# Performance work log

Measured on AMD Instinct MI355X. Metric: run time of the kernel, lower is better.

## Reference

```python
import jax, jax.numpy as jnp
import numpy as np

EPS = 1e-7
MAX_NORM = 1.0 - 1e-3  # projection radius of the unit Poincare ball (c=1)
ALPHA = 0.2            # LeakyReLU negative slope
NEG_INF = -9e15


def _proj(x, max_norm=MAX_NORM):
    # Project points back inside the Poincare ball along the last dim.
    norm = jnp.clip(jnp.linalg.norm(x, axis=-1, keepdims=True), EPS)
    return jnp.where(norm > max_norm, x / norm * max_norm, x)


def _logmap0(x):
    # Log map at the origin of the Poincare ball, c = 1.
    norm = jnp.clip(jnp.linalg.norm(x, axis=-1, keepdims=True), EPS, 1.0 - EPS)
    return jnp.arctanh(norm) * x / norm


def _expmap0(v):
    # Exp map at the origin of the Poincare ball, c = 1.
    norm = jnp.clip(jnp.linalg.norm(v, axis=-1, keepdims=True), EPS)
    return jnp.tanh(norm) * v / norm


def setup_inputs() -> dict:
    key = jax.random.key(0)
    k1, k2, k3 = jax.random.split(key, 3)
    N, D = 12288, 128
    # points strictly inside the ball: ||x|| ~ 0.01*sqrt(128) ~ 0.11 < 1
    x = jax.random.normal(k1, (N, D), dtype=jnp.float32) * 0.01
    adj = jax.random.randint(k2, (N, N), 0, 2, dtype=jnp.int32)
    # attention vector a, as in init: N(0, 0.2) then proj(a, 0.9) row-wise
    a = jax.random.normal(k3, (2 * D, 1), dtype=jnp.float32) * 0.2
    a = _proj(a, 0.9)
    return {"x": x, "adj": adj, "a": a}


def reference(x, adj, a):
    D = a.shape[0] // 2
    x_tan = _logmap0(x)                       # [N, D]
    wh1 = x_tan @ a[:D]                       # [N, 1]
    wh2 = x_tan @ a[D:]                       # [N, 1]
    e = jax.nn.leaky_relu(wh1 + wh2.T, ALPHA)  # [N, N] additive scores
    scores = jnp.where(adj > 0, e, NEG_INF)
    attention = jax.nn.softmax(scores, axis=1)  # dropout omitted (eval mode)
    x_tan_prime = attention @ x_tan            # [N, D]
    return _proj(_expmap0(x_tan_prime))
```

## Files before the change

kernel.cpp:

```cpp
#include <hip/hip_runtime.h>
#include <math.h>

#define NN 12288
#define DD 128
#define EPSF 1e-7f
#define MAXNORM (1.0f - 1e-3f)
#define S_SLABS 24

typedef __attribute__((ext_vector_type(8))) short short8_t;
typedef __attribute__((ext_vector_type(4))) float float4_t;
typedef unsigned short ushort_t;

__device__ __forceinline__ unsigned short f2bf(float f) {
    unsigned int u = __builtin_bit_cast(unsigned int, f);
    unsigned int r = u + 0x7FFFu + ((u >> 16) & 1u);
    return (unsigned short)(r >> 16);
}

__global__ __launch_bounds__(128) void prep_kernel(
    const float* __restrict__ x, const float* __restrict__ a,
    ushort_t* __restrict__ xtb,
    float* __restrict__ wh1, float* __restrict__ wh2)
{
    const int r = blockIdx.x;
    const int t = threadIdx.x;
    const float xv = x[r * DD + t];
    const float a1 = a[t];
    const float a2 = a[DD + t];
    float s0 = xv * xv, s1 = xv * a1, s2 = xv * a2;
    #pragma unroll
    for (int o = 32; o > 0; o >>= 1) {
        s0 += __shfl_xor(s0, o);
        s1 += __shfl_xor(s1, o);
        s2 += __shfl_xor(s2, o);
    }
    __shared__ float red[6];
    const int w = t >> 6;
    if ((t & 63) == 0) { red[w * 3 + 0] = s0; red[w * 3 + 1] = s1; red[w * 3 + 2] = s2; }
    __syncthreads();
    const float sumsq = red[0] + red[3];
    const float d1    = red[1] + red[4];
    const float d2    = red[2] + red[5];
    const float nraw  = sqrtf(sumsq);
    const float nrm   = fminf(fmaxf(nraw, EPSF), 1.0f - EPSF);
    const float scale = atanhf(nrm) / nrm;
    xtb[(size_t)r * DD + t] = f2bf(xv * scale);
    if (t == 0) {
        wh1[r] = scale * d1;
        wh2[r] = scale * d2;
    }
}

__global__ __launch_bounds__(256) void swizzle_kernel(
    const ushort_t* __restrict__ xtb, ushort_t* __restrict__ xtB)
{
    __shared__ ushort_t raw[32 * 136];
    const int C = blockIdx.x;
    const int t = threadIdx.x;
    #pragma unroll
    for (int p = 0; p < 2; ++p) {
        const int idx = p * 256 + t;
        const int j = idx >> 4, cell = idx & 15;
        const uint4 v = *(const uint4*)(xtb + (size_t)(C * 32 + j) * DD + cell * 8);
        *(uint4*)&raw[j * 136 + cell * 8] = v;
    }
    __syncthreads();
    #pragma unroll
    for (int p = 0; p < 2; ++p) {
        const int oc = p * 256 + t;
        const int dt = oc >> 6;
        const int l6 = oc & 63;
        const int l15 = l6 & 15, q = l6 >> 4;
        short8_t v;
        #pragma unroll
        for (int e = 0; e < 8; ++e)
            v[e] = (short)raw[(q * 8 + e) * 136 + dt * 16 + l15];
        *(short8_t*)(xtB + (size_t)C * 4096 + oc * 8) = v;
    }
}

__global__ __launch_bounds__(256, 1) void attn_kernel(
    const int* __restrict__ adj,
    const ushort_t* __restrict__ xtB,
    const float* __restrict__ wh1, const float* __restrict__ wh2,
    float* __restrict__ pout, float* __restrict__ plsum)
{
    __shared__ __align__(16) ushort_t B_lds[512 * DD];
    __shared__ __align__(16) float wh2_lds[512];

    const int t = threadIdx.x;
    const int w = t >> 6, lane = t & 63;
    const int l15 = lane & 15, quad = lane >> 4;
    const int s = blockIdx.y;
    const int jcol0 = s * 512;
    const int rowbase = blockIdx.x * 256 + w * 64;

    {
        const uint4* src = (const uint4*)(xtB + (size_t)(jcol0 >> 5) * 4096);
        uint4* dst = (uint4*)B_lds;
        #pragma unroll
        for (int m = 0; m < 32; ++m) dst[m * 256 + t] = src[m * 256 + t];
        wh2_lds[t]       = wh2[jcol0 + t];
        wh2_lds[256 + t] = wh2[jcol0 + 256 + t];
    }

    float wh1r[4];
    #pragma unroll
    for (int it = 0; it < 4; ++it) wh1r[it] = wh1[rowbase + it * 16 + l15];

    __syncthreads();

    const int* adj_lane = adj + (size_t)(rowbase + l15) * NN + jcol0 + quad * 8;

    float4_t acc[8];
    float lsum = 0.0f;
    int4 A0[8], A1[8], A2[8];

    auto load_step = [&](int st, int4 (&A)[8]) {
        const int it = st >> 2, jh = st & 3;
        const int* bp = adj_lane + (size_t)it * 16 * NN + jh * 128;
        #pragma unroll
        for (int kc = 0; kc < 4; ++kc) {
            A[kc * 2 + 0] = *(const int4*)(bp + kc * 32);
            A[kc * 2 + 1] = *(const int4*)(bp + kc * 32 + 4);
        }
    };

    auto process = [&](int st, int4 (&A)[8]) {
        const int it = st >> 2, jh = st & 3;
        if (jh == 0) {
            #pragma unroll
            for (int dt = 0; dt < 8; ++dt) acc[dt] = (float4_t)0.0f;
            lsum = 0.0f;
        }
        const float wh1i = wh1r[it];
        #pragma unroll
        for (int kc = 0; kc < 4; ++kc) {
            const int wbase = jh * 128 + kc * 32 + quad * 8;
            const float4 Wa = *(const float4*)&wh2_lds[wbase];
            const float4 Wb = *(const float4*)&wh2_lds[wbase + 4];
            const int4 Aa = A[kc * 2 + 0], Ac = A[kc * 2 + 1];
            const float u0 = wh1i + Wa.x, u1 = wh1i + Wa.y;
            const float u2 = wh1i + Wa.z, u3 = wh1i + Wa.w;
            const float u4 = wh1i + Wb.x, u5 = wh1i + Wb.y;
            const float u6 = wh1i + Wb.z, u7 = wh1i + Wb.w;
            const float p0 = (Aa.x > 0) ? __expf(fmaxf(u0, 0.2f * u0)) : 0.0f;
            const float p1 = (Aa.y > 0) ? __expf(fmaxf(u1, 0.2f * u1)) : 0.0f;
            const float p2 = (Aa.z > 0) ? __expf(fmaxf(u2, 0.2f * u2)) : 0.0f;
            const float p3 = (Aa.w > 0) ? __expf(fmaxf(u3, 0.2f * u3)) : 0.0f;
            const float p4 = (Ac.x > 0) ? __expf(fmaxf(u4, 0.2f * u4)) : 0.0f;
            const float p5 = (Ac.y > 0) ? __expf(fmaxf(u5, 0.2f * u5)) : 0.0f;
            const float p6 = (Ac.z > 0) ? __expf(fmaxf(u6, 0.2f * u6)) : 0.0f;
            const float p7 = (Ac.w > 0) ? __expf(fmaxf(u7, 0.2f * u7)) : 0.0f;
            lsum += ((p0 + p1) + (p2 + p3)) + ((p4 + p5) + (p6 + p7));
            short8_t af;
            af[0] = (short)f2bf(p0); af[1] = (short)f2bf(p1);
            af[2] = (short)f2bf(p2); af[3] = (short)f2bf(p3);
            af[4] = (short)f2bf(p4); af[5] = (short)f2bf(p5);
            af[6] = (short)f2bf(p6); af[7] = (short)f2bf(p7);
            const int cb = (jh * 4 + kc) * 4096;
            #pragma unroll
            for (int dt = 0; dt < 8; ++dt) {
                const short8_t Bf = *(const short8_t*)&B_lds[cb + dt * 512 + lane * 8];
                acc[dt] = __builtin_amdgcn_mfma_f32_16x16x32_bf16(af, Bf, acc[dt], 0, 0, 0);
            }
        }
        if (jh == 3) {
            float v = lsum;
            v += __shfl_xor(v, 16);
            v += __shfl_xor(v, 32);
            const int row0 = rowbase + it * 16;
            if (quad == 0) plsum[(size_t)s * NN + row0 + l15] = v;
            #pragma unroll
            for (int dt = 0; dt < 8; ++dt)
                #pragma unroll
                for (int reg = 0; reg < 4; ++reg)
                    pout[((size_t)s * NN + row0 + quad * 4 + reg) * DD + dt * 16 + l15]
                        = acc[dt][reg];
        }
    };

    load_step(0, A0);
    load_step(1, A1);
    #pragma unroll
    for (int st = 0; st < 16; ++st) {
        if (st + 2 < 16) {
            const int m2 = (st + 2) % 3;
            if (m2 == 0)      load_step(st + 2, A0);
            else if (m2 == 1) load_step(st + 2, A1);
            else              load_step(st + 2, A2);
        }
        const int m = st % 3;
        if (m == 0)      process(st, A0);
        else if (m == 1) process(st, A1);
        else             process(st, A2);
    }
}

__global__ __launch_bounds__(128) void reduce_kernel(
    const float* __restrict__ pout, const float* __restrict__ plsum,
    float* __restrict__ out)
{
    const int i = blockIdx.x;
    const int t = threadIdx.x;
    float v = 0.0f;
    for (int s = 0; s < S_SLABS; ++s) v += pout[((size_t)s * NN + i) * DD + t];
    float ls = 0.0f;
    for (int s = 0; s < S_SLABS; ++s) ls += plsum[(size_t)s * NN + i];
    v /= ls;
    float ss = v * v;
    #pragma unroll
    for (int o = 1; o < 64; o <<= 1) ss += __shfl_xor(ss, o);
    __shared__ float r2[2];
    if ((t & 63) == 0) r2[t >> 6] = ss;
    __syncthreads();
    const float total = r2[0] + r2[1];
    const float nraw = sqrtf(total);
    const float nv   = fmaxf(nraw, EPSF);
    const float th   = tanhf(nv);
    const float ysc  = th / nv;
    const float nyr  = ysc * nraw;
    const float ny   = fmaxf(nyr, EPSF);
    const float psc  = (ny > MAXNORM) ? (MAXNORM / ny) : 1.0f;
    const float os   = ysc * psc;
    out[(size_t)i * DD + t] = v * os;
}

extern "C" void kernel_launch(void* const* d_in, const int* in_sizes, int n_in,
                              void* d_out, int out_size, void* d_ws, size_t ws_size,
                              hipStream_t stream) {
    const float* x   = (const float*)d_in[0];
    const int*   adj = (const int*)d_in[1];
    const float* a   = (const float*)d_in[2];
    float* out = (float*)d_out;

    char* ws = (char*)d_ws;
    ushort_t* xtb = (ushort_t*)ws;  ws += (size_t)NN * DD * sizeof(ushort_t);
    ushort_t* xtB = (ushort_t*)ws;  ws += (size_t)NN * DD * sizeof(ushort_t);
    float* wh1 = (float*)ws;        ws += NN * sizeof(float);
    float* wh2 = (float*)ws;        ws += NN * sizeof(float);
    float* plsum = (float*)ws;      ws += (size_t)S_SLABS * NN * sizeof(float);
    float* pout  = (float*)ws;

    prep_kernel<<<NN, 128, 0, stream>>>(x, a, xtb, wh1, wh2);
    swizzle_kernel<<<NN / 32, 256, 0, stream>>>(xtb, xtB);
    attn_kernel<<<dim3(NN / 256, S_SLABS), 256, 0, stream>>>(
        adj, xtB, wh1, wh2, pout, plsum);
    reduce_kernel<<<NN, 128, 0, stream>>>(pout, plsum, out);
}
```

Baseline: 859.0 us.

## Pack adjacency into bitmask and restructure attention kernel over wider windows

Adds a pre-pass that compresses the int32 adjacency matrix into a bitmask with wave ballots, so the attention kernel reads bits instead of full ints. The attention kernel now keeps accumulators for all four row tiles across two 512-column windows and halves the number of column slabs, which cuts partial-output traffic and reduction work. It also preloads B fragments and wh2 values into registers per column chunk. The trade-offs are a separate full pass over adj, higher register pressure, and fewer blocks in the grid.

Result: slower. 1.212 ms (+41.1%).

```diff
diff --git a/kernel.cpp b/kernel.cpp
--- a/kernel.cpp
+++ b/kernel.cpp
@@ -5,7 +5,9 @@
 #define DD 128
 #define EPSF 1e-7f
 #define MAXNORM (1.0f - 1e-3f)
-#define S_SLABS 24
+#define S_SLABS 12
+#define JWIN 1024
+#define WROW 192
 
 typedef __attribute__((ext_vector_type(8))) short short8_t;
 typedef __attribute__((ext_vector_type(4))) float float4_t;
@@ -15,6 +17,27 @@
     unsigned int u = __builtin_bit_cast(unsigned int, f);
     unsigned int r = u + 0x7FFFu + ((u >> 16) & 1u);
     return (unsigned short)(r >> 16);
+}
+
+__global__ __launch_bounds__(256) void compress_kernel(
+    const int* __restrict__ adj, unsigned long long* __restrict__ bits)
+{
+    const int lane = threadIdx.x & 63;
+    const int wid  = (blockIdx.x * 256 + threadIdx.x) >> 6;
+    const int nw   = (gridDim.x * 256) >> 6;
+    const size_t total = (size_t)NN * NN / 256;
+    for (size_t itr = wid; itr < total; itr += nw) {
+        const size_t base = itr * 256;
+        unsigned long long m0, m1, m2, m3;
+        m0 = __ballot(adj[base +   0 + lane] > 0);
+        m1 = __ballot(adj[base +  64 + lane] > 0);
+        m2 = __ballot(adj[base + 128 + lane] > 0);
+        m3 = __ballot(adj[base + 192 + lane] > 0);
+        if (lane == 0) {
+            ulonglong4 o; o.x = m0; o.y = m1; o.z = m2; o.w = m3;
+            *(ulonglong4*)&bits[base >> 6] = o;
+        }
+    }
 }
 
 __global__ __launch_bounds__(128) void prep_kernel(
@@ -80,7 +103,7 @@
 }
 
 __global__ __launch_bounds__(256, 1) void attn_kernel(
-    const int* __restrict__ adj,
+    const unsigned int* __restrict__ bits,
     const ushort_t* __restrict__ xtB,
     const float* __restrict__ wh1, const float* __restrict__ wh2,
     float* __restrict__ pout, float* __restrict__ plsum)
@@ -92,108 +115,103 @@
     const int w = t >> 6, lane = t & 63;
     const int l15 = lane & 15, quad = lane >> 4;
     const int s = blockIdx.y;
-    const int jcol0 = s * 512;
     const int rowbase = blockIdx.x * 256 + w * 64;
 
-    {
-        const uint4* src = (const uint4*)(xtB + (size_t)(jcol0 >> 5) * 4096);
-        uint4* dst = (uint4*)B_lds;
-        #pragma unroll
-        for (int m = 0; m < 32; ++m) dst[m * 256 + t] = src[m * 256 + t];
-        wh2_lds[t]       = wh2[jcol0 + t];
-        wh2_lds[256 + t] = wh2[jcol0 + 256 + t];
-    }
-
     float wh1r[4];
     #pragma unroll
     for (int it = 0; it < 4; ++it) wh1r[it] = wh1[rowbase + it * 16 + l15];
 
-    __syncthreads();
-
-    const int* adj_lane = adj + (size_t)(rowbase + l15) * NN + jcol0 + quad * 8;
-
-    float4_t acc[8];
-    float lsum = 0.0f;
-    int4 A0[8], A1[8], A2[8];
-
-    auto load_step = [&](int st, int4 (&A)[8]) {
-        const int it = st >> 2, jh = st & 3;
-        const int* bp = adj_lane + (size_t)it * 16 * NN + jh * 128;
-        #pragma unroll
-        for (int kc = 0; kc < 4; ++kc) {
-            A[kc * 2 + 0] = *(const int4*)(bp + kc * 32);
-            A[kc * 2 + 1] = *(const int4*)(bp + kc * 32 + 4);
+    float4_t acc[4][8];
+    #pragma unroll
+    for (int it = 0; it < 4; ++it)
+        #pragma unroll
+        for (int dt = 0; dt < 8; ++dt) acc[it][dt] = (float4_t)0.0f;
+    float lsum[4] = {0.0f, 0.0f, 0.0f, 0.0f};
+
+    for (int win = 0; win < 2; ++win) {
+        const int jcol0 = s * JWIN + win * 512;
+        if (win) __syncthreads();
+        {
+            const uint4* src = (const uint4*)(xtB + (size_t)(jcol0 >> 5) * 4096);
+            uint4* dst = (uint4*)B_lds;
+            #pragma unroll
+            for (int m = 0; m < 32; ++m) dst[m * 256 + t] = src[m * 256 + t];
+            wh2_lds[t]       = wh2[jcol0 + t];
+            wh2_lds[256 + t] = wh2[jcol0 + 256 + t];
         }
-    };
-
-    auto process = [&](int st, int4 (&A)[8]) {
-        const int it = st >> 2, jh = st & 3;
-        if (jh == 0) {
-            #pragma unroll
-            for (int dt = 0; dt < 8; ++dt) acc[dt] = (float4_t)0.0f;
-            lsum = 0.0f;
-        }
-        const float wh1i = wh1r[it];
-        #pragma unroll
-        for (int kc = 0; kc < 4; ++kc) {
-            const int wbase = jh * 128 + kc * 32 + quad * 8;
-            const float4 Wa = *(const float4*)&wh2_lds[wbase];
-            const float4 Wb = *(const float4*)&wh2_lds[wbase + 4];
-            const int4 Aa = A[kc * 2 + 0], Ac = A[kc * 2 + 1];
-            const float u0 = wh1i + Wa.x, u1 = wh1i + Wa.y;
-            const float u2 = wh1i + Wa.z, u3 = wh1i + Wa.w;
-            const float u4 = wh1i + Wb.x, u5 = wh1i + Wb.y;
-            const float u6 = wh1i + Wb.z, u7 = wh1i + Wb.w;
-            const float p0 = (Aa.x > 0) ? __expf(fmaxf(u0, 0.2f * u0)) : 0.0f;
-            const float p1 = (Aa.y > 0) ? __expf(fmaxf(u1, 0.2f * u1)) : 0.0f;
-            const float p2 = (Aa.z > 0) ? __expf(fmaxf(u2, 0.2f * u2)) : 0.0f;
-            const float p3 = (Aa.w > 0) ? __expf(fmaxf(u3, 0.2f * u3)) : 0.0f;
-            const float p4 = (Ac.x > 0) ? __expf(fmaxf(u4, 0.2f * u4)) : 0.0f;
-            const float p5 = (Ac.y > 0) ? __expf(fmaxf(u5, 0.2f * u5)) : 0.0f;
-            const float p6 = (Ac.z > 0) ? __expf(fmaxf(u6, 0.2f * u6)) : 0.0f;
-            const float p7 = (Ac.w > 0) ? __expf(fmaxf(u7, 0.2f * u7)) : 0.0f;
-            lsum += ((p0 + p1) + (p2 + p3)) + ((p4 + p5) + (p6 + p7));
-            short8_t af;
-            af[0] = (short)f2bf(p0); af[1] = (short)f2bf(p1);
-            af[2] = (short)f2bf(p2); af[3] = (short)f2bf(p3);
-            af[4] = (short)f2bf(p4); af[5] = (short)f2bf(p5);
-            af[6] = (short)f2bf(p6); af[7] = (short)f2bf(p7);
-            const int cb = (jh * 4 + kc) * 4096;
-            #pragma unroll
-            for (int dt = 0; dt < 8; ++dt) {
-                const short8_t Bf = *(const short8_t*)&B_lds[cb + dt * 512 + lane * 8];
-                acc[dt] = __builtin_amdgcn_mfma_f32_16x16x32_bf16(af, Bf, acc[dt], 0, 0, 0);
+        __syncthreads();
+
+        #pragma unroll
+        for (int jh = 0; jh < 4; ++jh) {
+            uint4 bw[4];
+            #pragma unroll
+            for (int it = 0; it < 4; ++it) {
+                const int row = rowbase + it * 16 + l15;
+                bw[it] = *(const uint4*)(bits + (size_t)row * (WROW * 2)
+                                         + (jcol0 >> 5) + jh * 4);
+            }
+            short8_t Bf[4][8];
+            #pragma unroll
+            for (int kc = 0; kc < 4; ++kc)
+                #pragma unroll
+                for (int dt = 0; dt < 8; ++dt)
+                    Bf[kc][dt] = *(const short8_t*)
+                        &B_lds[(jh * 4 + kc) * 4096 + dt * 512 + lane * 8];
+            float4 Wa[4], Wb[4];
+            #pragma unroll
+            for (int kc = 0; kc < 4; ++kc) {
+                const int wb = jh * 128 + kc * 32 + quad * 8;
+                Wa[kc] = *(const float4*)&wh2_lds[wb];
+                Wb[kc] = *(const float4*)&wh2_lds[wb + 4];
+            }
+
+            #pragma unroll
+            for (int it = 0; it < 4; ++it) {
+                const float wh1i = wh1r[it];
+                const unsigned wk[4] = {bw[it].x, bw[it].y, bw[it].z, bw[it].w};
+                #pragma unroll
+                for (int kc = 0; kc < 4; ++kc) {
+                    const unsigned byte = (wk[kc] >> (quad * 8)) & 0xffu;
+                    const float u0 = wh1i + Wa[kc].x, u1 = wh1i + Wa[kc].y;
+                    const float u2 = wh1i + Wa[kc].z, u3 = wh1i + Wa[kc].w;
+                    const float u4 = wh1i + Wb[kc].x, u5 = wh1i + Wb[kc].y;
+                    const float u6 = wh1i + Wb[kc].z, u7 = wh1i + Wb[kc].w;
+                    const float p0 = (byte & 1u)   ? __expf(fmaxf(u0, 0.2f * u0)) : 0.0f;
+                    const float p1 = (byte & 2u)   ? __expf(fmaxf(u1, 0.2f * u1)) : 0.0f;
+                    const float p2 = (byte & 4u)   ? __expf(fmaxf(u2, 0.2f * u2)) : 0.0f;
+                    const float p3 = (byte & 8u)   ? __expf(fmaxf(u3, 0.2f * u3)) : 0.0f;
+                    const float p4 = (byte & 16u)  ? __expf(fmaxf(u4, 0.2f * u4)) : 0.0f;
+                    const float p5 = (byte & 32u)  ? __expf(fmaxf(u5, 0.2f * u5)) : 0.0f;
+                    const float p6 = (byte & 64u)  ? __expf(fmaxf(u6, 0.2f * u6)) : 0.0f;
+                    const float p7 = (byte & 128u) ? __expf(fmaxf(u7, 0.2f * u7)) : 0.0f;
+                    lsum[it] += ((p0 + p1) + (p2 + p3)) + ((p4 + p5) + (p6 + p7));
+                    short8_t af;
+                    af[0] = (short)f2bf(p0); af[1] = (short)f2bf(p1);
+                    af[2] = (short)f2bf(p2); af[3] = (short)f2bf(p3);
+                    af[4] = (short)f2bf(p4); af[5] = (short)f2bf(p5);
+                    af[6] = (short)f2bf(p6); af[7] = (short)f2bf(p7);
+                    #pragma unroll
+                    for (int dt = 0; dt < 8; ++dt)
+                        acc[it][dt] = __builtin_amdgcn_mfma_f32_16x16x32_bf16(
+                            af, Bf[kc][dt], acc[it][dt], 0, 0, 0);
+                }
             }
         }
-        if (jh == 3) {
-            float v = lsum;
-            v += __shfl_xor(v, 16);
-            v += __shfl_xor(v, 32);
-            const int row0 = rowbase + it * 16;
-            if (quad == 0) plsum[(size_t)s * NN + row0 + l15] = v;
-            #pragma unroll
-            for (int dt = 0; dt < 8; ++dt)
-                #pragma unroll
-                for (int reg = 0; reg < 4; ++reg)
-                    pout[((size_t)s * NN + row0 + quad * 4 + reg) * DD + dt * 16 + l15]
-                        = acc[dt][reg];
-        }
-    };
-
-    load_step(0, A0);
-    load_step(1, A1);
-    #pragma unroll
-    for (int st = 0; st < 16; ++st) {
-        if (st + 2 < 16) {
-            const int m2 = (st + 2) % 3;
-            if (m2 == 0)      load_step(st + 2, A0);
-            else if (m2 == 1) load_step(st + 2, A1);
-            else              load_step(st + 2, A2);
-        }
-        const int m = st % 3;
-        if (m == 0)      process(st, A0);
-        else if (m == 1) process(st, A1);
-        else             process(st, A2);
+    }
+
+    #pragma unroll
+    for (int it = 0; it < 4; ++it) {
+        float v = lsum[it];
+        v += __shfl_xor(v, 16);
+        v += __shfl_xor(v, 32);
+        const int row0 = rowbase + it * 16;
+        if (quad == 0) plsum[(size_t)s * NN + row0 + l15] = v;
+        #pragma unroll
+        for (int dt = 0; dt < 8; ++dt)
+            #pragma unroll
+            for (int reg = 0; reg < 4; ++reg)
+                pout[((size_t)s * NN + row0 + quad * 4 + reg) * DD + dt * 16 + l15]
+                    = acc[it][dt][reg];
     }
 }
 
@@ -204,8 +222,10 @@
     const int i = blockIdx.x;
     const int t = threadIdx.x;
     float v = 0.0f;
+    #pragma unroll
     for (int s = 0; s < S_SLABS; ++s) v += pout[((size_t)s * NN + i) * DD + t];
     float ls = 0.0f;
+    #pragma unroll
     for (int s = 0; s < S_SLABS; ++s) ls += plsum[(size_t)s * NN + i];
     v /= ls;
     float ss = v * v;
@@ -235,6 +255,8 @@
     float* out = (float*)d_out;
 
     char* ws = (char*)d_ws;
+    unsigned long long* bits = (unsigned long long*)ws;
+    ws += (size_t)NN * WROW * sizeof(unsigned long long);
     ushort_t* xtb = (ushort_t*)ws;  ws += (size_t)NN * DD * sizeof(ushort_t);
     ushort_t* xtB = (ushort_t*)ws;  ws += (size_t)NN * DD * sizeof(ushort_t);
     float* wh1 = (float*)ws;        ws += NN * sizeof(float);
@@ -242,9 +264,10 @@
     float* plsum = (float*)ws;      ws += (size_t)S_SLABS * NN * sizeof(float);
     float* pout  = (float*)ws;
 
+    compress_kernel<<<2048, 256, 0, stream>>>(adj, bits);
     prep_kernel<<<NN, 128, 0, stream>>>(x, a, xtb, wh1, wh2);
     swizzle_kernel<<<NN / 32, 256, 0, stream>>>(xtb, xtB);
     attn_kernel<<<dim3(NN / 256, S_SLABS), 256, 0, stream>>>(
-        adj, xtB, wh1, wh2, pout, plsum);
+        (const unsigned int*)bits, xtB, wh1, wh2, pout, plsum);
     reduce_kernel<<<NN, 128, 0, stream>>>(pout, plsum, out);
 }
```
